# Kernel tuning notes

Measured on AMD Instinct MI355X. Metric: run time of the kernel, lower is better.

## Reference

```python
import jax, jax.numpy as jnp
import numpy as np

NUM_HEADS = 16
HEAD_DIM = 64
D_MODEL = 1024
B, L = 8, 4096


def _relative_position_encoding(seq_len, dim):
    positions = jnp.arange(seq_len, dtype=jnp.float32)[:, None]
    div_term = jnp.exp(jnp.arange(0, dim, 2, dtype=jnp.float32) * (-(np.log(10000.0) / dim)))
    ang = positions * div_term  # [L, dim//2]
    pe = jnp.zeros((seq_len, dim), dtype=jnp.float32)
    pe = pe.at[:, 0::2].set(jnp.sin(ang))
    pe = pe.at[:, 1::2].set(jnp.cos(ang))
    return pe


def setup_inputs() -> dict:
    key = jax.random.key(0)
    k1, k2, k3 = jax.random.split(key, 3)
    x = jax.random.normal(k1, (B, L, D_MODEL), dtype=jnp.float32)
    w_qkv = jax.random.normal(k2, (D_MODEL, 3 * NUM_HEADS * HEAD_DIM), dtype=jnp.float32) * (1.0 / np.sqrt(D_MODEL))
    b_qkv = jnp.zeros((3 * NUM_HEADS * HEAD_DIM,), dtype=jnp.float32)
    w_out = jax.random.normal(k3, (NUM_HEADS * HEAD_DIM, D_MODEL), dtype=jnp.float32) * (1.0 / np.sqrt(NUM_HEADS * HEAD_DIM))
    b_out = jnp.zeros((D_MODEL,), dtype=jnp.float32)
    return {"x": x, "w_qkv": w_qkv, "b_qkv": b_qkv, "w_out": w_out, "b_out": b_out}


def reference(x, w_qkv, b_qkv, w_out, b_out):
    Bq, Lq, _ = x.shape
    qkv = x @ w_qkv + b_qkv                              # [B, L, 3*H*Dh]
    qkv = qkv.reshape(Bq, Lq, NUM_HEADS, 3 * HEAD_DIM)   # [B, L, H, 3*Dh]
    q, k, v = jnp.split(qkv, 3, axis=-1)                 # each [B, L, H, Dh]
    pos_enc = _relative_position_encoding(Lq, HEAD_DIM)  # [L, Dh]
    k = k + pos_enc[None, :, None, :]
    scale = jnp.sqrt(jnp.float32(HEAD_DIM))
    # NOTE: faithful to source -- contraction over head_dim with batch dims (B, L):
    # attention matrix is [B, L, H, H] (across heads, not sequence).
    attn = jnp.einsum('blhd,bl gd->blhg'.replace(' ', ''), q, k) / scale  # [B, L, H, H]
    attn = jax.nn.softmax(attn, axis=-1)
    out = jnp.einsum('blhg,blgd->blhd', attn, v)          # [B, L, H, Dh]
    out = out.reshape(Bq, Lq, NUM_HEADS * HEAD_DIM)
    return out @ w_out + b_out
```

## Files before the change

kernel.cpp:

```cpp
#include <hip/hip_runtime.h>
#include <hip/hip_bf16.h>
#include <cstdint>
#include <cstddef>

#define NH   16
#define DHD  64
#define DM   1024
#define BSZ  8
#define SEQ  4096
#define NTOK (BSZ*SEQ)
#define NQKV (3*NH*DHD)

typedef __attribute__((ext_vector_type(8))) __bf16 bf16x8;
typedef __attribute__((ext_vector_type(4))) float  floatx4;

static __device__ __forceinline__ unsigned short f2bf(float f) {
    unsigned int u = __float_as_uint(f);
    u += 0x7fffu + ((u >> 16) & 1u);
    return (unsigned short)(u >> 16);
}
static __device__ __forceinline__ float bf2f(unsigned int us) {
    return __uint_as_float(us << 16);
}
static __device__ __forceinline__ void load_lds16(const void* g, void* l) {
    __builtin_amdgcn_global_load_lds((__attribute__((address_space(1))) void*)g,
                                     (__attribute__((address_space(3))) void*)l,
                                     16, 0, 0);
}

__global__ __launch_bounds__(256) void k_cast_bf16(const float* __restrict__ in,
                                                   unsigned short* __restrict__ out, int n4) {
    int i = blockIdx.x * 256 + threadIdx.x;
    if (i >= n4) return;
    float4 v = ((const float4*)in)[i];
    ushort4 o;
    o.x = f2bf(v.x); o.y = f2bf(v.y); o.z = f2bf(v.z); o.w = f2bf(v.w);
    ((ushort4*)out)[i] = o;
}

template<int R, int C>
__global__ __launch_bounds__(256) void k_transpose_cast(const float* __restrict__ in,
                                                        unsigned short* __restrict__ out) {
    __shared__ float tile[32][33];
    int tx = threadIdx.x, ty = threadIdx.y;
    int col = blockIdx.x * 32 + tx;
#pragma unroll
    for (int k = 0; k < 4; k++) {
        int row = blockIdx.y * 32 + ty + k * 8;
        tile[ty + k * 8][tx] = in[(size_t)row * C + col];
    }
    __syncthreads();
#pragma unroll
    for (int k = 0; k < 4; k++) {
        int ocol = blockIdx.x * 32 + ty + k * 8;
        int orow = blockIdx.y * 32 + tx;
        out[(size_t)ocol * R + orow] = f2bf(tile[tx][ty + k * 8]);
    }
}

__global__ __launch_bounds__(256) void k_pe(float* __restrict__ pe) {
    int t = blockIdx.x * 256 + threadIdx.x;
    int l = t >> 5, i = t & 31;
    float dv = expf(-0.14391156831212787f * (float)(2 * i));
    float ang = (float)l * dv;
    pe[l * 64 + 2 * i]     = sinf(ang);
    pe[l * 64 + 2 * i + 1] = cosf(ang);
}

template<int N, int EPI>
__global__ __launch_bounds__(256) void k_gemm(const unsigned short* __restrict__ A,
                                              const unsigned short* __restrict__ BT,
                                              const float* __restrict__ bias,
                                              const float* __restrict__ pe,
                                              void* __restrict__ Cout) {
    constexpr int K = 1024;
    __shared__ __align__(16) short lds[8192];
    short* As = lds;
    short* Bs = lds + 4096;

    int tid  = threadIdx.x;
    int lane = tid & 63;
    int wid  = tid >> 6;
    int m0 = blockIdx.y * 128;
    int n0 = blockIdx.x * 128;
    int wr = wid >> 1, wc = wid & 1;
    int l15 = lane & 15;
    int kq  = (lane >> 4) * 8;

    floatx4 acc[4][4];
#pragma unroll
    for (int i = 0; i < 4; i++)
#pragma unroll
        for (int j = 0; j < 4; j++) acc[i][j] = (floatx4){0.f, 0.f, 0.f, 0.f};

    int ci0 = wid * 128 + lane;
    int ci1 = ci0 + 64;
    const unsigned short* pa0 = A  + (size_t)(m0 + (ci0 >> 2)) * K + (ci0 & 3) * 8;
    const unsigned short* pa1 = A  + (size_t)(m0 + (ci1 >> 2)) * K + (ci1 & 3) * 8;
    const unsigned short* pb0 = BT + (size_t)(n0 + (ci0 >> 2)) * K + (ci0 & 3) * 8;
    const unsigned short* pb1 = BT + (size_t)(n0 + (ci1 >> 2)) * K + (ci1 & 3) * 8;
    short* la0 = As + ci0 * 8;
    short* la1 = As + ci1 * 8;
    short* lb0 = Bs + ci0 * 8;
    short* lb1 = Bs + ci1 * 8;

    for (int kb = 0; kb < K; kb += 32) {
        __syncthreads();
        load_lds16(pa0 + kb, la0);
        load_lds16(pa1 + kb, la1);
        load_lds16(pb0 + kb, lb0);
        load_lds16(pb1 + kb, lb1);
        __syncthreads();

        bf16x8 aF[4], bF[4];
#pragma unroll
        for (int i = 0; i < 4; i++)
            aF[i] = *(const bf16x8*)&As[(wr * 64 + i * 16 + l15) * 32 + kq];
#pragma unroll
        for (int j = 0; j < 4; j++)
            bF[j] = *(const bf16x8*)&Bs[(wc * 64 + j * 16 + l15) * 32 + kq];
#pragma unroll
        for (int i = 0; i < 4; i++)
#pragma unroll
            for (int j = 0; j < 4; j++)
                acc[i][j] = __builtin_amdgcn_mfma_f32_16x16x32_bf16(aF[i], bF[j], acc[i][j], 0, 0, 0);
    }

    int rbase = (lane >> 4) * 4;
#pragma unroll
    for (int j = 0; j < 4; j++) {
        int col = n0 + wc * 64 + j * 16 + l15;
        float bv = bias[col];
        int h = 0, rc = 0;
        if (EPI == 1) { h = col / 192; rc = col - h * 192; }
#pragma unroll
        for (int i = 0; i < 4; i++) {
#pragma unroll
            for (int r = 0; r < 4; r++) {
                int row = m0 + wr * 64 + i * 16 + rbase + r;
                float v = acc[i][j][r] + bv;
                if (EPI == 1) {
                    if (rc < 64)        v *= 0.125f;
                    else if (rc < 128)  v += pe[(row & (SEQ - 1)) * 64 + (rc - 64)];
                    ((unsigned short*)Cout)[(size_t)row * N + col] = f2bf(v);
                } else {
                    ((float*)Cout)[(size_t)row * N + col] = v;
                }
            }
        }
    }
}

__global__ __launch_bounds__(256) void k_attn(const unsigned short* __restrict__ qkv,
                                              unsigned short* __restrict__ aout) {
    __shared__ __align__(16) float X4[4][3264];
    __shared__ float S4[4][272];
    int tid = threadIdx.x, wid = tid >> 6, lane = tid & 63;
    int t = blockIdx.x * 4 + wid;

    float* X = X4[wid];
    const unsigned short* src = qkv + (size_t)t * NQKV;

#pragma unroll
    for (int c = 0; c < 6; c++) {
        int ci = c * 64 + lane;
        uint4 u = ((const uint4*)src)[ci];
        int j0 = ci * 8;
        int h  = j0 / 192;
        int rc = j0 - h * 192;
        float* dst = X + h * 204 + rc;
        floatx4 f0 = { bf2f(u.x & 0xffff), bf2f(u.x >> 16), bf2f(u.y & 0xffff), bf2f(u.y >> 16) };
        floatx4 f1 = { bf2f(u.z & 0xffff), bf2f(u.z >> 16), bf2f(u.w & 0xffff), bf2f(u.w >> 16) };
        *(floatx4*)dst       = f0;
        *(floatx4*)(dst + 4) = f1;
    }
    __syncthreads();

    int h  = lane >> 2;
    int g0 = (lane & 3) * 4;
    const float* Q = X + h * 204;
    float s0 = 0.f, s1 = 0.f, s2 = 0.f, s3 = 0.f;
#pragma unroll 8
    for (int d = 0; d < 64; d++) {
        float qd = Q[d];
        s0 += qd * X[(g0 + 0) * 204 + 64 + d];
        s1 += qd * X[(g0 + 1) * 204 + 64 + d];
        s2 += qd * X[(g0 + 2) * 204 + 64 + d];
        s3 += qd * X[(g0 + 3) * 204 + 64 + d];
    }
    float mx = fmaxf(fmaxf(s0, s1), fmaxf(s2, s3));
    mx = fmaxf(mx, __shfl_xor(mx, 1));
    mx = fmaxf(mx, __shfl_xor(mx, 2));
    float e0 = __expf(s0 - mx), e1 = __expf(s1 - mx), e2 = __expf(s2 - mx), e3 = __expf(s3 - mx);
    float sum = e0 + e1 + e2 + e3;
    sum += __shfl_xor(sum, 1);
    sum += __shfl_xor(sum, 2);
    float inv = 1.0f / sum;
    float* Sr = &S4[wid][h * 17];
    Sr[g0 + 0] = e0 * inv; Sr[g0 + 1] = e1 * inv; Sr[g0 + 2] = e2 * inv; Sr[g0 + 3] = e3 * inv;
    __syncthreads();

    int db = lane & 3;
    floatx4 o0 = {0,0,0,0}, o1 = {0,0,0,0}, o2 = {0,0,0,0}, o3 = {0,0,0,0};
    const float* Sh = &S4[wid][h * 17];
#pragma unroll
    for (int g = 0; g < 16; g++) {
        float p = Sh[g];
        const floatx4* Vg = (const floatx4*)(X + g * 204 + 128 + db * 16);
        o0 += Vg[0] * p;
        o1 += Vg[1] * p;
        o2 += Vg[2] * p;
        o3 += Vg[3] * p;
    }
    unsigned int w[8];
    w[0] = (unsigned)f2bf(o0[0]) | ((unsigned)f2bf(o0[1]) << 16);
    w[1] = (unsigned)f2bf(o0[2]) | ((unsigned)f2bf(o0[3]) << 16);
    w[2] = (unsigned)f2bf(o1[0]) | ((unsigned)f2bf(o1[1]) << 16);
    w[3] = (unsigned)f2bf(o1[2]) | ((unsigned)f2bf(o1[3]) << 16);
    w[4] = (unsigned)f2bf(o2[0]) | ((unsigned)f2bf(o2[1]) << 16);
    w[5] = (unsigned)f2bf(o2[2]) | ((unsigned)f2bf(o2[3]) << 16);
    w[6] = (unsigned)f2bf(o3[0]) | ((unsigned)f2bf(o3[1]) << 16);
    w[7] = (unsigned)f2bf(o3[2]) | ((unsigned)f2bf(o3[3]) << 16);
    uint4* dst = (uint4*)&aout[(size_t)t * DM + h * 64 + db * 16];
    dst[0] = make_uint4(w[0], w[1], w[2], w[3]);
    dst[1] = make_uint4(w[4], w[5], w[6], w[7]);
}

extern "C" void kernel_launch(void* const* d_in, const int* in_sizes, int n_in,
                              void* d_out, int out_size, void* d_ws, size_t ws_size,
                              hipStream_t stream) {
    const float* x     = (const float*)d_in[0];
    const float* w_qkv = (const float*)d_in[1];
    const float* b_qkv = (const float*)d_in[2];
    const float* w_out = (const float*)d_in[3];
    const float* b_out = (const float*)d_in[4];
    float* out = (float*)d_out;

    char* ws = (char*)d_ws;
    float*          pe    = (float*)ws;
    unsigned short* wqkvT = (unsigned short*)(ws + (1u << 20));
    unsigned short* woutT = (unsigned short*)(ws + (1u << 20) + 6291456u);
    unsigned short* xbf   = (unsigned short*)(ws + (1u << 20) + 6291456u + 2097152u);
    unsigned short* qkv   = (unsigned short*)(ws + (1u << 20) + 6291456u + 2097152u + 67108864u);
    unsigned short* aout  = xbf;

    k_cast_bf16<<<(NTOK * DM / 4 + 255) / 256, 256, 0, stream>>>(x, xbf, NTOK * DM / 4);
    k_transpose_cast<1024, 3072><<<dim3(96, 32), dim3(32, 8), 0, stream>>>(w_qkv, wqkvT);
    k_transpose_cast<1024, 1024><<<dim3(32, 32), dim3(32, 8), 0, stream>>>(w_out, woutT);
    k_pe<<<512, 256, 0, stream>>>(pe);

    k_gemm<NQKV, 1><<<dim3(NQKV / 128, NTOK / 128), 256, 0, stream>>>(xbf, wqkvT, b_qkv, pe, qkv);

    k_attn<<<NTOK / 4, 256, 0, stream>>>(qkv, aout);

    k_gemm<DM, 0><<<dim3(DM / 128, NTOK / 128), 256, 0, stream>>>(aout, woutT, b_out, nullptr, out);
}
```

Before: 735.9 us.

## Use MFMA for per-token head attention and stage QKV GEMM epilogue through LDS

The per-token 16x16 head attention now computes QK^T with bf16 MFMA and P·V with f16 MFMA, replacing scalar FMA loops over an fp32 LDS copy. V and the probabilities are staged into LDS as f16, and the softmax reductions use cross-lane shuffles. The QKV GEMM epilogue writes bf16 results into a swizzled LDS tile so each thread can emit 16-byte coalesced global stores instead of scattered 2-byte stores. Exchanges: extra syncthreads and LDS traffic in the epilogue, and f16 rounding of probabilities and V.

```diff
diff --git a/kernel.cpp b/kernel.cpp
--- a/kernel.cpp
+++ b/kernel.cpp
@@ -13,6 +13,7 @@
 
 typedef __attribute__((ext_vector_type(8))) __bf16 bf16x8;
 typedef __attribute__((ext_vector_type(4))) float  floatx4;
+typedef __attribute__((ext_vector_type(4))) _Float16 f16x4;
 
 static __device__ __forceinline__ unsigned short f2bf(float f) {
     unsigned int u = __float_as_uint(f);
@@ -21,6 +22,10 @@
 }
 static __device__ __forceinline__ float bf2f(unsigned int us) {
     return __uint_as_float(us << 16);
+}
+static __device__ __forceinline__ unsigned short f2h(float f) {
+    _Float16 h = (_Float16)f;
+    return __builtin_bit_cast(unsigned short, h);
 }
 static __device__ __forceinline__ void load_lds16(const void* g, void* l) {
     __builtin_amdgcn_global_load_lds((__attribute__((address_space(1))) void*)g,
@@ -74,7 +79,7 @@
                                               const float* __restrict__ pe,
                                               void* __restrict__ Cout) {
     constexpr int K = 1024;
-    __shared__ __align__(16) short lds[8192];
+    __shared__ __align__(16) short lds[8704];
     short* As = lds;
     short* Bs = lds + 4096;
 
@@ -85,7 +90,8 @@
     int n0 = blockIdx.x * 128;
     int wr = wid >> 1, wc = wid & 1;
     int l15 = lane & 15;
-    int kq  = (lane >> 4) * 8;
+    int quad = lane >> 4;
+    int kq  = quad * 8;
 
     floatx4 acc[4][4];
 #pragma unroll
@@ -126,104 +132,145 @@
                 acc[i][j] = __builtin_amdgcn_mfma_f32_16x16x32_bf16(aF[i], bF[j], acc[i][j], 0, 0, 0);
     }
 
-    int rbase = (lane >> 4) * 4;
-#pragma unroll
-    for (int j = 0; j < 4; j++) {
-        int col = n0 + wc * 64 + j * 16 + l15;
-        float bv = bias[col];
-        int h = 0, rc = 0;
-        if (EPI == 1) { h = col / 192; rc = col - h * 192; }
-#pragma unroll
-        for (int i = 0; i < 4; i++) {
-#pragma unroll
-            for (int r = 0; r < 4; r++) {
-                int row = m0 + wr * 64 + i * 16 + rbase + r;
-                float v = acc[i][j][r] + bv;
-                if (EPI == 1) {
-                    if (rc < 64)        v *= 0.125f;
-                    else if (rc < 128)  v += pe[(row & (SEQ - 1)) * 64 + (rc - 64)];
-                    ((unsigned short*)Cout)[(size_t)row * N + col] = f2bf(v);
-                } else {
-                    ((float*)Cout)[(size_t)row * N + col] = v;
+    if (EPI == 1) {
+        short* T = lds;
+        __syncthreads();
+#pragma unroll
+        for (int p = 0; p < 2; p++) {
+            if (wr == p) {
+#pragma unroll
+                for (int j = 0; j < 4; j++) {
+                    int col = n0 + wc * 64 + j * 16 + l15;
+                    float bv = bias[col];
+                    int h = col / 192, rc = col - h * 192;
+                    int csw = (wc * 64 + j * 16 + l15) ^ (quad << 3);
+#pragma unroll
+                    for (int i = 0; i < 4; i++) {
+#pragma unroll
+                        for (int r = 0; r < 4; r++) {
+                            int rl = i * 16 + quad * 4 + r;
+                            int row = m0 + p * 64 + rl;
+                            float v = acc[i][j][r] + bv;
+                            if (rc < 64)       v *= 0.125f;
+                            else if (rc < 128) v += pe[(row & (SEQ - 1)) * 64 + (rc - 64)];
+                            T[rl * 136 + csw] = (short)f2bf(v);
+                        }
+                    }
                 }
             }
+            __syncthreads();
+            {
+                int rl = tid >> 2, coff = (tid & 3) * 32;
+                int sw = ((rl >> 2) & 3) * 8;
+                unsigned short* dst = (unsigned short*)Cout + (size_t)(m0 + p * 64 + rl) * N + n0 + coff;
+#pragma unroll
+                for (int k = 0; k < 4; k++) {
+                    uint4 u = *(const uint4*)&T[rl * 136 + ((coff + k * 8) ^ sw)];
+                    *(uint4*)(dst + k * 8) = u;
+                }
+            }
+            __syncthreads();
+        }
+    } else {
+        int rbase = quad * 4;
+#pragma unroll
+        for (int j = 0; j < 4; j++) {
+            int col = n0 + wc * 64 + j * 16 + l15;
+            float bv = bias[col];
+#pragma unroll
+            for (int i = 0; i < 4; i++) {
+#pragma unroll
+                for (int r = 0; r < 4; r++) {
+                    int row = m0 + wr * 64 + i * 16 + rbase + r;
+                    ((float*)Cout)[(size_t)row * N + col] = acc[i][j][r] + bv;
+                }
+            }
         }
     }
 }
 
 __global__ __launch_bounds__(256) void k_attn(const unsigned short* __restrict__ qkv,
                                               unsigned short* __restrict__ aout) {
-    __shared__ __align__(16) float X4[4][3264];
-    __shared__ float S4[4][272];
+    __shared__ __align__(16) unsigned short lds[4][2752];
     int tid = threadIdx.x, wid = tid >> 6, lane = tid & 63;
+    unsigned short* VT = lds[wid];
+    unsigned short* PL = VT + 1280;
+    unsigned short* OL = PL + 320;
     int t = blockIdx.x * 4 + wid;
-
-    float* X = X4[wid];
-    const unsigned short* src = qkv + (size_t)t * NQKV;
-
-#pragma unroll
-    for (int c = 0; c < 6; c++) {
-        int ci = c * 64 + lane;
-        uint4 u = ((const uint4*)src)[ci];
-        int j0 = ci * 8;
-        int h  = j0 / 192;
-        int rc = j0 - h * 192;
-        float* dst = X + h * 204 + rc;
-        floatx4 f0 = { bf2f(u.x & 0xffff), bf2f(u.x >> 16), bf2f(u.y & 0xffff), bf2f(u.y >> 16) };
-        floatx4 f1 = { bf2f(u.z & 0xffff), bf2f(u.z >> 16), bf2f(u.w & 0xffff), bf2f(u.w >> 16) };
-        *(floatx4*)dst       = f0;
-        *(floatx4*)(dst + 4) = f1;
-    }
-    __syncthreads();
-
-    int h  = lane >> 2;
-    int g0 = (lane & 3) * 4;
-    const float* Q = X + h * 204;
-    float s0 = 0.f, s1 = 0.f, s2 = 0.f, s3 = 0.f;
-#pragma unroll 8
-    for (int d = 0; d < 64; d++) {
-        float qd = Q[d];
-        s0 += qd * X[(g0 + 0) * 204 + 64 + d];
-        s1 += qd * X[(g0 + 1) * 204 + 64 + d];
-        s2 += qd * X[(g0 + 2) * 204 + 64 + d];
-        s3 += qd * X[(g0 + 3) * 204 + 64 + d];
-    }
-    float mx = fmaxf(fmaxf(s0, s1), fmaxf(s2, s3));
-    mx = fmaxf(mx, __shfl_xor(mx, 1));
-    mx = fmaxf(mx, __shfl_xor(mx, 2));
-    float e0 = __expf(s0 - mx), e1 = __expf(s1 - mx), e2 = __expf(s2 - mx), e3 = __expf(s3 - mx);
-    float sum = e0 + e1 + e2 + e3;
-    sum += __shfl_xor(sum, 1);
-    sum += __shfl_xor(sum, 2);
-    float inv = 1.0f / sum;
-    float* Sr = &S4[wid][h * 17];
-    Sr[g0 + 0] = e0 * inv; Sr[g0 + 1] = e1 * inv; Sr[g0 + 2] = e2 * inv; Sr[g0 + 3] = e3 * inv;
-    __syncthreads();
-
-    int db = lane & 3;
-    floatx4 o0 = {0,0,0,0}, o1 = {0,0,0,0}, o2 = {0,0,0,0}, o3 = {0,0,0,0};
-    const float* Sh = &S4[wid][h * 17];
-#pragma unroll
-    for (int g = 0; g < 16; g++) {
-        float p = Sh[g];
-        const floatx4* Vg = (const floatx4*)(X + g * 204 + 128 + db * 16);
-        o0 += Vg[0] * p;
-        o1 += Vg[1] * p;
-        o2 += Vg[2] * p;
-        o3 += Vg[3] * p;
-    }
-    unsigned int w[8];
-    w[0] = (unsigned)f2bf(o0[0]) | ((unsigned)f2bf(o0[1]) << 16);
-    w[1] = (unsigned)f2bf(o0[2]) | ((unsigned)f2bf(o0[3]) << 16);
-    w[2] = (unsigned)f2bf(o1[0]) | ((unsigned)f2bf(o1[1]) << 16);
-    w[3] = (unsigned)f2bf(o1[2]) | ((unsigned)f2bf(o1[3]) << 16);
-    w[4] = (unsigned)f2bf(o2[0]) | ((unsigned)f2bf(o2[1]) << 16);
-    w[5] = (unsigned)f2bf(o2[2]) | ((unsigned)f2bf(o2[3]) << 16);
-    w[6] = (unsigned)f2bf(o3[0]) | ((unsigned)f2bf(o3[1]) << 16);
-    w[7] = (unsigned)f2bf(o3[2]) | ((unsigned)f2bf(o3[3]) << 16);
-    uint4* dst = (uint4*)&aout[(size_t)t * DM + h * 64 + db * 16];
-    dst[0] = make_uint4(w[0], w[1], w[2], w[3]);
-    dst[1] = make_uint4(w[4], w[5], w[6], w[7]);
+    int l15 = lane & 15, q = lane >> 4;
+
+    const unsigned short* rowp = qkv + (size_t)t * NQKV + l15 * 192 + q * 8;
+
+    bf16x8 aQ0 = *(const bf16x8*)(rowp);
+    bf16x8 bK0 = *(const bf16x8*)(rowp + 64);
+    bf16x8 aQ1 = *(const bf16x8*)(rowp + 32);
+    bf16x8 bK1 = *(const bf16x8*)(rowp + 96);
+    uint4  v0  = *(const uint4*)(rowp + 128);
+    uint4  v1  = *(const uint4*)(rowp + 160);
+
+    floatx4 S = {0.f, 0.f, 0.f, 0.f};
+    S = __builtin_amdgcn_mfma_f32_16x16x32_bf16(aQ0, bK0, S, 0, 0, 0);
+    S = __builtin_amdgcn_mfma_f32_16x16x32_bf16(aQ1, bK1, S, 0, 0, 0);
+
+    {
+        unsigned int w0[4] = {v0.x, v0.y, v0.z, v0.w};
+        unsigned int w1[4] = {v1.x, v1.y, v1.z, v1.w};
+#pragma unroll
+        for (int i = 0; i < 4; i++) {
+            int d = q * 8 + 2 * i;
+            VT[(d)      * 20 + l15] = f2h(bf2f(w0[i] & 0xffff));
+            VT[(d + 1)  * 20 + l15] = f2h(bf2f(w0[i] >> 16));
+            VT[(d + 32) * 20 + l15] = f2h(bf2f(w1[i] & 0xffff));
+            VT[(d + 33) * 20 + l15] = f2h(bf2f(w1[i] >> 16));
+        }
+    }
+
+    float e0, e1, e2, e3, i0, i1, i2, i3;
+    {
+        float m0 = S[0], m1 = S[1], m2 = S[2], m3 = S[3];
+#pragma unroll
+        for (int d = 1; d < 16; d <<= 1) {
+            m0 = fmaxf(m0, __shfl_xor(m0, d));
+            m1 = fmaxf(m1, __shfl_xor(m1, d));
+            m2 = fmaxf(m2, __shfl_xor(m2, d));
+            m3 = fmaxf(m3, __shfl_xor(m3, d));
+        }
+        e0 = __expf(S[0] - m0); e1 = __expf(S[1] - m1);
+        e2 = __expf(S[2] - m2); e3 = __expf(S[3] - m3);
+        float s0 = e0, s1 = e1, s2 = e2, s3 = e3;
+#pragma unroll
+        for (int d = 1; d < 16; d <<= 1) {
+            s0 += __shfl_xor(s0, d); s1 += __shfl_xor(s1, d);
+            s2 += __shfl_xor(s2, d); s3 += __shfl_xor(s3, d);
+        }
+        i0 = 1.f / s0; i1 = 1.f / s1; i2 = 1.f / s2; i3 = 1.f / s3;
+    }
+    PL[(q * 4 + 0) * 20 + l15] = f2h(e0);
+    PL[(q * 4 + 1) * 20 + l15] = f2h(e1);
+    PL[(q * 4 + 2) * 20 + l15] = f2h(e2);
+    PL[(q * 4 + 3) * 20 + l15] = f2h(e3);
+
+    f16x4 aP = *(const f16x4*)&PL[l15 * 20 + q * 4];
+    floatx4 O[4];
+#pragma unroll
+    for (int c = 0; c < 4; c++) {
+        f16x4 bV = *(const f16x4*)&VT[(c * 16 + l15) * 20 + q * 4];
+        O[c] = __builtin_amdgcn_mfma_f32_16x16x16f16(aP, bV, (floatx4){0.f, 0.f, 0.f, 0.f}, 0, 0, 0);
+    }
+
+    float inv[4] = {i0, i1, i2, i3};
+#pragma unroll
+    for (int c = 0; c < 4; c++)
+#pragma unroll
+        for (int r = 0; r < 4; r++)
+            OL[(q * 4 + r) * 72 + c * 16 + l15] = f2bf(O[c][r] * inv[r]);
+
+    int h2 = lane >> 2, a = lane & 3;
+    uint4 o0 = *(const uint4*)&OL[h2 * 72 + a * 16];
+    uint4 o1 = *(const uint4*)&OL[h2 * 72 + a * 16 + 8];
+    uint4* dst = (uint4*)&aout[(size_t)t * DM + lane * 16];
+    dst[0] = o0;
+    dst[1] = o1;
 }
 
 extern "C" void kernel_launch(void* const* d_in, const int* in_sizes, int n_in,
@@ -250,8 +297,6 @@
     k_pe<<<512, 256, 0, stream>>>(pe);
 
     k_gemm<NQKV, 1><<<dim3(NQKV / 128, NTOK / 128), 256, 0, stream>>>(xbf, wqkvT, b_qkv, pe, qkv);
-
     k_attn<<<NTOK / 4, 256, 0, stream>>>(qkv, aout);
-
     k_gemm<DM, 0><<<dim3(DM / 128, NTOK / 128), 256, 0, stream>>>(aout, woutT, b_out, nullptr, out);
 }
```

Result: slower. 791.9 us (+7.6%).
